# Optimization experiments

Measured on AMD Instinct MI355X. Metric: run time of the kernel, lower is better.

## Reference

```python
import jax, jax.numpy as jnp
import numpy as np

SHIFTS = (1, 2)          # _GLOBAL_SHIFTS, all < channels so none filtered
LN_EPS = 1e-5


def _layernorm(x, g, b):
    mu = jnp.mean(x, axis=-1, keepdims=True)
    var = jnp.var(x, axis=-1, keepdims=True)
    return (x - mu) * jax.lax.rsqrt(var + LN_EPS) * g + b


def setup_inputs() -> dict:
    key = jax.random.key(0)
    ks = jax.random.split(key, 4)
    B, H, W, D = 8, 96, 96, 256
    n_comp = 2 * len(SHIFTS)  # full mode: dot + wedge per shift
    x = jax.random.normal(ks[0], (B, H, W, D), dtype=jnp.float32)
    # glorot-uniform style scaling for the two dense kernels
    pk = jax.random.normal(ks[1], (n_comp * D, D), dtype=jnp.float32) * (1.0 / np.sqrt(n_comp * D))
    gk = jax.random.normal(ks[2], (2 * D, D), dtype=jnp.float32) * (1.0 / np.sqrt(2 * D))
    return {
        "x": x,
        "ln_gamma": jnp.ones((D,), jnp.float32),
        "ln_beta": jnp.zeros((D,), jnp.float32),
        "proj_kernel": pk,
        "proj_bias": jnp.zeros((D,), jnp.float32),
        "gate_kernel": gk,
        "gate_bias": jnp.zeros((D,), jnp.float32),
        "gamma": jnp.full((D,), 1e-5, jnp.float32),  # LayerScale init
    }


def reference(x, ln_gamma, ln_beta, proj_kernel, proj_bias,
              gate_kernel, gate_bias, gamma):
    # ---- pre-norm ----
    h_norm = _layernorm(x, ln_gamma, ln_beta)                 # [B,H,W,D]
    # ---- context stream (ctx_mode='diff'): deviation from spatial mean ----
    z_det = h_norm
    z_ctx = h_norm - jnp.mean(h_norm, axis=(1, 2), keepdims=True)
    # ---- sparse rolling Clifford product (cli_mode='full') ----
    feats = []
    for s in SHIFTS:
        ctx_s = jnp.roll(z_ctx, -s, axis=-1)   # Z_ctx[(c+s) % D]
        det_s = jnp.roll(z_det, -s, axis=-1)   # Z_det[(c+s) % D]
        dot = jax.nn.silu(z_det * ctx_s)                      # inner part
        wedge = z_det * ctx_s - z_ctx * det_s                 # bivector part
        feats.append(dot)
        feats.append(wedge)
    feats = jnp.concatenate(feats, axis=-1)                   # [B,H,W,4D]
    g_feat = feats @ proj_kernel + proj_bias                  # [B,H,W,D]
    # ---- gated geometric residual ----
    gate_in = jnp.concatenate([h_norm, g_feat], axis=-1)      # [B,H,W,2D]
    alpha = jax.nn.sigmoid(gate_in @ gate_kernel + gate_bias)
    h_mix = (jax.nn.silu(h_norm) + alpha * g_feat) * gamma    # LayerScale
    # drop_path_rate == 0.0 -> identity; caller-side residual add
    return x + h_mix
```

## Files before the change

### kernel.cpp

```cpp
#include <hip/hip_runtime.h>
#include <hip/hip_bf16.h>

typedef unsigned short u16;
typedef unsigned int   u32;
typedef __attribute__((ext_vector_type(2))) float f32x2;
typedef __attribute__((ext_vector_type(4))) float f32x4;
typedef __attribute__((ext_vector_type(4))) u32   u32x4;
typedef __attribute__((ext_vector_type(8))) short bf16x8;

#define HWPIX  9216
#define NPIX   73728
#define LN_EPS 1e-5f
#define MROW   64
#define ASTR   40

template<int N> struct IC { static constexpr int value = N; };

__device__ __forceinline__ u16 f2bf(float f){
  u32 u = __builtin_bit_cast(u32, f);
  u += 0x7fffu + ((u >> 16) & 1u);
  return (u16)(u >> 16);
}
__device__ __forceinline__ u32 pkbf(float lo, float hi){
  u32 d;
  asm("v_cvt_pk_bf16_f32 %0, %1, %2" : "=v"(d) : "v"(lo), "v"(hi));
  return d;
}
__device__ __forceinline__ float bfu2f(u16 h){ return __builtin_bit_cast(float, (u32)h << 16); }
__device__ __forceinline__ float fsigmoid(float v){ return __fdividef(1.f, 1.f + __expf(-v)); }
__device__ __forceinline__ float fsilu(float v){ return __fdividef(v, 1.f + __expf(-v)); }

__device__ __forceinline__ void gld16(const u16* g, u16* l){
  __builtin_amdgcn_global_load_lds((const __attribute__((address_space(1))) void*)g,
                                   (__attribute__((address_space(3))) void*)l,
                                   16, 0, 0);
}

__global__ __launch_bounds__(256) void wconv(const float* __restrict__ pk,
                                             const float* __restrict__ gk,
                                             u16* __restrict__ wsdot,
                                             u16* __restrict__ wsgate)
{
  int gid = blockIdx.x * 256 + threadIdx.x;
  int t = gid >> 10, S = gid & 1023;
  int q = (S >> 2) & 15, pp = S & 3, w8 = (S >> 6) & 7, rb = S >> 9;
  int n  = rb * 128 + w8 * 16 + q;
  int kq = pp ^ ((q >> 1) & 3);
  const float* W; int k0; u16* dst;
  if (t < 16) { W = pk; k0 = (t & 1) * 512 + (t >> 1) * 32 + kq * 8; dst = wsdot + (size_t)t * 8192; }
  else        { W = gk; k0 = (t - 16) * 32 + kq * 8;                 dst = wsgate + (size_t)(t - 16) * 8192; }
  u32 ow[4];
  #pragma unroll
  for (int e = 0; e < 4; ++e) {
    float f0 = W[(size_t)(k0 + 2*e)     * 256 + n];
    float f1 = W[(size_t)(k0 + 2*e + 1) * 256 + n];
    ow[e] = (u32)f2bf(f0) | ((u32)f2bf(f1) << 16);
  }
  *(u32x4*)(dst + (size_t)S * 8) = (u32x4){ow[0], ow[1], ow[2], ow[3]};
}

__global__ __launch_bounds__(256) void prep(const float* __restrict__ x,
                                            const float* __restrict__ g,
                                            const float* __restrict__ bt,
                                            float* __restrict__ mu_rs,
                                            float* __restrict__ partial)
{
  const int bh = blockIdx.x;
  const int tid = threadIdx.x;
  const int wv = tid >> 6, lane = tid & 63;
  const float* xrow = x + (size_t)bh * 96 * 256;
  __shared__ float red[4][256];

  f32x4 gv = *(const f32x4*)(g  + lane * 4);
  f32x4 bv = *(const f32x4*)(bt + lane * 4);
  f32x4 acc = {0.f, 0.f, 0.f, 0.f};

  for (int w = wv; w < 96; w += 4) {
    f32x4 v = *(const f32x4*)(xrow + w * 256 + lane * 4);
    float s  = v[0] + v[1] + v[2] + v[3];
    float s2 = v[0]*v[0] + v[1]*v[1] + v[2]*v[2] + v[3]*v[3];
    #pragma unroll
    for (int m = 1; m < 64; m <<= 1) { s += __shfl_xor(s, m); s2 += __shfl_xor(s2, m); }
    float mu  = s * (1.f / 256.f);
    float var = s2 * (1.f / 256.f) - mu * mu;
    float rs  = rsqrtf(var + LN_EPS);
    if (lane == 0) *(f32x2*)(mu_rs + (size_t)(bh * 96 + w) * 2) = f32x2{mu, rs};
    #pragma unroll
    for (int j = 0; j < 4; ++j) acc[j] += (v[j] - mu) * rs * gv[j] + bv[j];
  }
  *(f32x4*)(&red[wv][lane * 4]) = acc;
  __syncthreads();
  float s = red[0][tid] + red[1][tid] + red[2][tid] + red[3][tid];
  partial[(size_t)bh * 256 + tid] = s;
}

__global__ __launch_bounds__(256) void ln_mean(const float* __restrict__ partial,
                                               float* __restrict__ mean)
{
  int b = blockIdx.x, c = threadIdx.x;
  float s = 0.f;
  for (int h = 0; h < 96; ++h) s += partial[((size_t)b * 96 + h) * 256 + c];
  float m = s * (1.f / 9216.f);
  mean[b * 258 + c] = m;
  if (c < 2) mean[b * 258 + 256 + c] = m;
}

__global__ __launch_bounds__(256) void wfold(const float* __restrict__ pk,
                                             const float* __restrict__ meang,
                                             u16* __restrict__ wsW)
{
  __shared__ float msh[256];
  int gid = blockIdx.x * 256 + threadIdx.x;
  int chunk = gid >> 10;
  int b = chunk >> 3, j = chunk & 7;
  msh[threadIdx.x] = meang[b * 258 + threadIdx.x];
  __syncthreads();
  int S = gid & 1023;
  int q = (S >> 2) & 15, pp = S & 3, w8 = (S >> 6) & 7, rb = S >> 9;
  int n  = rb * 128 + w8 * 16 + q;
  int kq = pp ^ ((q >> 1) & 3);
  u32 ow[4];
  #pragma unroll
  for (int e = 0; e < 4; ++e) {
    float r[2];
    #pragma unroll
    for (int hh = 0; hh < 2; ++hh) {
      int c = j * 32 + kq * 8 + 2 * e + hh;
      int cm1 = (c + 255) & 255, cm2 = (c + 254) & 255;
      int cp1 = (c + 1) & 255,   cp2 = (c + 2) & 255;
      r[hh] = msh[cm1] * pk[(size_t)(256 + cm1) * 256 + n]
            - msh[cp1] * pk[(size_t)(256 + c)   * 256 + n]
            + msh[cm2] * pk[(size_t)(768 + cm2) * 256 + n]
            - msh[cp2] * pk[(size_t)(768 + c)   * 256 + n];
    }
    ow[e] = (u32)f2bf(r[0]) | ((u32)f2bf(r[1]) << 16);
  }
  *(u32x4*)(wsW + (size_t)chunk * 8192 + (size_t)S * 8) = (u32x4){ow[0], ow[1], ow[2], ow[3]};
}

__global__ __launch_bounds__(512, 2) void fused(
    const float* __restrict__ x,
    const float* __restrict__ lng, const float* __restrict__ lnb,
    const u16* __restrict__ wsdot, const u16* __restrict__ wsW,
    const u16* __restrict__ wsgate, const float* __restrict__ mu_rs,
    const float* __restrict__ pbias, const float* __restrict__ gbias,
    const float* __restrict__ gamma, const float* __restrict__ meang,
    float* __restrict__ out)
{
  __shared__ u16 afg[2][MROW * ASTR];
  __shared__ u16 Bl [4][8192];
  __shared__ float gshb[2][260];
  __shared__ float msh[258];
  __shared__ float mursh[128];

  const int tid  = threadIdx.x;
  const long pix0 = (long)blockIdx.x * MROW;
  const int bat  = (int)(pix0 / HWPIX);

  const int wave = tid >> 6, lane = tid & 63;
  const int wr = wave & 1, wc = wave >> 1;
  const int fr = lane & 15, kq = lane >> 4;
  const int bswz = (kq ^ ((fr >> 1) & 3)) * 8;
  const int brow = tid >> 3, o4 = (tid & 7) * 4;

  auto stageQ = [&](auto QC) {
    constexpr int q = decltype(QC)::value;
    constexpr int sl = q & 3;
    const u16* base;
    if constexpr (q < 32) {
      constexpr int w = q >> 2, r = q & 3;
      if constexpr      (r == 0) base = wsdot  + (size_t)(2 * w)     * 8192;
      else if constexpr (r == 1) base = wsdot  + (size_t)(2 * w + 1) * 8192;
      else if constexpr (r == 2) base = wsW + (size_t)bat * 65536 + (size_t)w * 8192;
      else                       base = wsgate + (size_t)w * 8192;
    } else {
      base = wsgate + (size_t)(q - 24) * 8192;
    }
    const u16* src = base + tid * 8;
    u16* dst = &Bl[sl][wave * 512];
    gld16(src, dst);
    gld16(src + 4096, dst + 4096);
  };

  stageQ(IC<0>{});
  stageQ(IC<1>{});

  if (tid < 256)      { gshb[0][tid] = lng[tid]; gshb[1][tid] = lnb[tid]; }
  else if (tid < 260) { int c = tid - 256; gshb[0][256 + c] = lng[c]; gshb[1][256 + c] = lnb[c]; }
  if (tid < 258) msh[tid] = meang[bat * 258 + tid];
  if (tid < 128) mursh[tid] = mu_rs[pix0 * 2 + tid];

  f32x4 accG[2][4], accA[2][4];
  #pragma unroll
  for (int i = 0; i < 2; ++i)
    #pragma unroll
    for (int j = 0; j < 4; ++j) { accG[i][j] = (f32x4){0,0,0,0}; accA[i][j] = (f32x4){0,0,0,0}; }
  u32 gfp[2][4][2];
  float pbv[4];
  #pragma unroll
  for (int nt = 0; nt < 4; ++nt) pbv[nt] = pbias[wc * 64 + nt * 16 + fr];

  __syncthreads();

  const float* xrowp = x + (pix0 + brow) * 256;
  const float muv = mursh[brow * 2];
  const float rsv = mursh[brow * 2 + 1];

  float h0, h1, h2, h3, h4, h5;
  auto computeH = [&](int w) {
    const int cc = w * 32 + o4;
    f32x4 xa = *(const f32x4*)(xrowp + cc);
    f32x2 xb = (cc == 252) ? f32x2{xrowp[0], xrowp[1]}
                           : *(const f32x2*)(xrowp + cc + 4);
    h0 = (xa[0] - muv) * rsv * gshb[0][cc]     + gshb[1][cc];
    h1 = (xa[1] - muv) * rsv * gshb[0][cc + 1] + gshb[1][cc + 1];
    h2 = (xa[2] - muv) * rsv * gshb[0][cc + 2] + gshb[1][cc + 2];
    h3 = (xa[3] - muv) * rsv * gshb[0][cc + 3] + gshb[1][cc + 3];
    h4 = (xb[0] - muv) * rsv * gshb[0][cc + 4] + gshb[1][cc + 4];
    h5 = (xb[1] - muv) * rsv * gshb[0][cc + 5] + gshb[1][cc + 5];
  };
  auto buildDot = [&](auto SC, int w, int buf) {
    constexpr int s = decltype(SC)::value;
    const int cc = w * 32 + o4;
    float a0, a1, a2, a3;
    if constexpr (s == 1) { a0 = h1; a1 = h2; a2 = h3; a3 = h4; }
    else                  { a0 = h2; a1 = h3; a2 = h4; a3 = h5; }
    float r0 = fsilu(h0 * (a0 - msh[cc + s]));
    float r1 = fsilu(h1 * (a1 - msh[cc + 1 + s]));
    float r2 = fsilu(h2 * (a2 - msh[cc + 2 + s]));
    float r3 = fsilu(h3 * (a3 - msh[cc + 3 + s]));
    *(u32*)(&afg[buf][brow * ASTR + o4])     = pkbf(r0, r1);
    *(u32*)(&afg[buf][brow * ASTR + o4 + 2]) = pkbf(r2, r3);
  };
  auto buildH = [&](int buf) {
    *(u32*)(&afg[buf][brow * ASTR + o4])     = pkbf(h0, h1);
    *(u32*)(&afg[buf][brow * ASTR + o4 + 2]) = pkbf(h2, h3);
  };
  auto gfcopy = [&](auto CGC, int buf) {
    constexpr int cg = decltype(CGC)::value;
    constexpr int par = cg & 1;
    if (wc == (cg >> 1)) {
      #pragma unroll
      for (int v = 0; v < 2; ++v) {
        #pragma unroll
        for (int ai = 0; ai < 2; ++ai)
          #pragma unroll
          for (int rp = 0; rp < 2; ++rp) {
            u32 pw = gfp[ai][par * 2 + v][rp];
            int row0 = wr * 32 + ai * 16 + kq * 4 + rp * 2;
            afg[buf][row0 * ASTR + v * 16 + fr]       = (u16)pw;
            afg[buf][(row0 + 1) * ASTR + v * 16 + fr] = (u16)(pw >> 16);
          }
      }
    }
  };

  auto mfma_into = [&](f32x4 (&ac)[2][4], int abuf, const u16* bp) {
    const u16* ar = &afg[abuf][(wr * 32 + fr) * ASTR + kq * 8];
    bf16x8 av0 = *(const bf16x8*)(ar);
    bf16x8 av1 = *(const bf16x8*)(ar + 16 * ASTR);
    __builtin_amdgcn_s_setprio(1);
    #pragma unroll
    for (int nt = 0; nt < 4; ++nt) {
      bf16x8 bv = *(const bf16x8*)(bp + nt * 512);
      ac[0][nt] = __builtin_amdgcn_mfma_f32_16x16x32_bf16(av0, bv, ac[0][nt], 0, 0, 0);
      ac[1][nt] = __builtin_amdgcn_mfma_f32_16x16x32_bf16(av1, bv, ac[1][nt], 0, 0, 0);
    }
    __builtin_amdgcn_s_setprio(0);
  };

  computeH(0);
  buildDot(IC<1>{}, 0, 0);
  asm volatile("s_waitcnt lgkmcnt(0)" ::: "memory");
  __builtin_amdgcn_s_barrier();

  auto stepfn = [&](auto TC) {
    constexpr int t = decltype(TC)::value;
    constexpr int u = t + 1;
    if constexpr (u < 24) {
      constexpr int r3 = u % 3, w = u / 3;
      if constexpr (r3 == 0)      { computeH(w); buildDot(IC<1>{}, w, u & 1); }
      else if constexpr (r3 == 1) buildDot(IC<2>{}, u / 3, u & 1);
      else                        buildH(u & 1);
    } else if constexpr (u >= 25 && u < 32) {
      gfcopy(IC<u - 24>{}, u & 1);
    }
    if constexpr (t < 24) {
      constexpr int g = t / 3, r3 = t % 3;
      if constexpr (r3 < 2) {
        constexpr int q = 4 * g + r3;
        mfma_into(accG, t & 1, &Bl[q & 3][wc * 2048 + fr * 32 + bswz]);
      } else {
        constexpr int q = 4 * g + 2;
        mfma_into(accG, t & 1, &Bl[q & 3][wc * 2048 + fr * 32 + bswz]);
        mfma_into(accA, t & 1, &Bl[(q + 1) & 3][wc * 2048 + fr * 32 + bswz]);
      }
    } else {
      constexpr int q = t + 8;
      mfma_into(accA, t & 1, &Bl[q & 3][wc * 2048 + fr * 32 + bswz]);
    }
    if constexpr (t == 23) {
      #pragma unroll
      for (int nt = 0; nt < 4; ++nt)
        #pragma unroll
        for (int ai = 0; ai < 2; ++ai) {
          f32x4 a = accG[ai][nt];
          gfp[ai][nt][0] = pkbf(a[0] + pbv[nt], a[1] + pbv[nt]);
          gfp[ai][nt][1] = pkbf(a[2] + pbv[nt], a[3] + pbv[nt]);
        }
      gfcopy(IC<0>{}, 0);
    }
    if constexpr (t + 2 < 32) {
      constexpr int s2 = t + 2;
      constexpr int nq = (s2 < 24) ? ((s2 % 3 == 2) ? 2 : 1) : 1;
      constexpr int q0 = (s2 < 24) ? (4 * (s2 / 3) + s2 % 3) : (s2 + 8);
      stageQ(IC<q0>{});
      if constexpr (nq == 2) {
        stageQ(IC<q0 + 1>{});
        asm volatile("s_waitcnt vmcnt(4) lgkmcnt(0)" ::: "memory");
      } else {
        asm volatile("s_waitcnt vmcnt(2) lgkmcnt(0)" ::: "memory");
      }
    } else {
      asm volatile("s_waitcnt vmcnt(0) lgkmcnt(0)" ::: "memory");
    }
    __builtin_amdgcn_s_barrier();
  };
  auto run8 = [&](auto B8) {
    constexpr int b8 = decltype(B8)::value;
    stepfn(IC<b8 + 0>{}); stepfn(IC<b8 + 1>{}); stepfn(IC<b8 + 2>{}); stepfn(IC<b8 + 3>{});
    stepfn(IC<b8 + 4>{}); stepfn(IC<b8 + 5>{}); stepfn(IC<b8 + 6>{}); stepfn(IC<b8 + 7>{});
  };
  run8(IC<0>{}); run8(IC<8>{}); run8(IC<16>{}); run8(IC<24>{});

  float gbv[4], gmv[4];
  #pragma unroll
  for (int nt = 0; nt < 4; ++nt) {
    int col = wc * 64 + nt * 16 + fr;
    gbv[nt] = gbias[col]; gmv[nt] = gamma[col];
  }
  #pragma unroll
  for (int ai = 0; ai < 2; ++ai)
    #pragma unroll
    for (int rr = 0; rr < 4; ++rr) {
      const int row = wr * 32 + ai * 16 + kq * 4 + rr;
      const long pix = pix0 + row;
      const float mu2 = mursh[row * 2], rs2 = mursh[row * 2 + 1];
      #pragma unroll
      for (int nt = 0; nt < 4; ++nt) {
        int col = wc * 64 + nt * 16 + fr;
        float xv = x[pix * 256 + col];
        float hh = (xv - mu2) * rs2 * gshb[0][col] + gshb[1][col];
        u32 pw = gfp[ai][nt][rr >> 1];
        float gfv = bfu2f((u16)((rr & 1) ? (pw >> 16) : pw));
        float al = fsigmoid(accA[ai][nt][rr] + gbv[nt]);
        out[pix * 256 + col] = xv + (fsilu(hh) + al * gfv) * gmv[nt];
      }
    }
}

extern "C" void kernel_launch(void* const* d_in, const int* in_sizes, int n_in,
                              void* d_out, int out_size, void* d_ws, size_t ws_size,
                              hipStream_t stream) {
  const float* x     = (const float*)d_in[0];
  const float* lng   = (const float*)d_in[1];
  const float* lnb   = (const float*)d_in[2];
  const float* pk    = (const float*)d_in[3];
  const float* pbias = (const float*)d_in[4];
  const float* gk    = (const float*)d_in[5];
  const float* gbias = (const float*)d_in[6];
  const float* gamma = (const float*)d_in[7];
  float* out = (float*)d_out;

  char* ws = (char*)d_ws;
  u16*   wsdot   = (u16*)ws;
  u16*   wsgate  = (u16*)(ws + 262144);
  float* meang   = (float*)(ws + 524288);
  u16*   wsW     = (u16*)(ws + 532544);
  float* partial = (float*)(ws + 532544);
  float* mu_rs   = (float*)(ws + 1581120);

  wconv<<<128, 256, 0, stream>>>(pk, gk, wsdot, wsgate);
  prep<<<768, 256, 0, stream>>>(x, lng, lnb, mu_rs, partial);
  ln_mean<<<8, 256, 0, stream>>>(partial, meang);
  wfold<<<256, 256, 0, stream>>>(pk, meang, wsW);
  fused<<<NPIX / MROW, 512, 0, stream>>>(x, lng, lnb, wsdot, wsW, wsgate, mu_rs,
                                         pbias, gbias, gamma, meang, out);
}
```

Baseline: 164.0 us.

## Reorder GEMM K-loop into uniform one-chunk steps with a triple-buffered weight ring

The fused K-loop is restructured so that every step stages and consumes exactly one 8192-element weight chunk. All dot chunks run first, then alternating wedge/gate-h chunks, then the remaining gate chunks. The LDS weight ring shrinks from four slots to three, and the step count grows from 32 to 40 with a uniform vmcnt(2) wait. Because channel chunks are now visited twice, the LayerNorm values for the gate-h chunks are recomputed from x via a new computeH4. This adds extra global reads and more barriers in exchange for a simpler, lower-LDS pipeline.

```diff
diff --git a/kernel.cpp b/kernel.cpp
--- a/kernel.cpp
+++ b/kernel.cpp
@@ -148,7 +148,7 @@
     float* __restrict__ out)
 {
   __shared__ u16 afg[2][MROW * ASTR];
-  __shared__ u16 Bl [4][8192];
+  __shared__ u16 Bl [3][8192];
   __shared__ float gshb[2][260];
   __shared__ float msh[258];
   __shared__ float mursh[128];
@@ -164,15 +164,15 @@
   const int brow = tid >> 3, o4 = (tid & 7) * 4;
 
   auto stageQ = [&](auto QC) {
-    constexpr int q = decltype(QC)::value;
-    constexpr int sl = q & 3;
+    constexpr int q  = decltype(QC)::value;
+    constexpr int sl = q % 3;
     const u16* base;
-    if constexpr (q < 32) {
-      constexpr int w = q >> 2, r = q & 3;
-      if constexpr      (r == 0) base = wsdot  + (size_t)(2 * w)     * 8192;
-      else if constexpr (r == 1) base = wsdot  + (size_t)(2 * w + 1) * 8192;
-      else if constexpr (r == 2) base = wsW + (size_t)bat * 65536 + (size_t)w * 8192;
-      else                       base = wsgate + (size_t)w * 8192;
+    if constexpr (q < 16) {
+      base = wsdot + (size_t)q * 8192;
+    } else if constexpr (q < 32) {
+      constexpr int p = q - 16, w = p >> 1;
+      if constexpr ((p & 1) == 0) base = wsW + (size_t)bat * 65536 + (size_t)w * 8192;
+      else                        base = wsgate + (size_t)w * 8192;
     } else {
       base = wsgate + (size_t)(q - 24) * 8192;
     }
@@ -196,9 +196,6 @@
     #pragma unroll
     for (int j = 0; j < 4; ++j) { accG[i][j] = (f32x4){0,0,0,0}; accA[i][j] = (f32x4){0,0,0,0}; }
   u32 gfp[2][4][2];
-  float pbv[4];
-  #pragma unroll
-  for (int nt = 0; nt < 4; ++nt) pbv[nt] = pbias[wc * 64 + nt * 16 + fr];
 
   __syncthreads();
 
@@ -207,7 +204,7 @@
   const float rsv = mursh[brow * 2 + 1];
 
   float h0, h1, h2, h3, h4, h5;
-  auto computeH = [&](int w) {
+  auto computeH6 = [&](int w) {
     const int cc = w * 32 + o4;
     f32x4 xa = *(const f32x4*)(xrowp + cc);
     f32x2 xb = (cc == 252) ? f32x2{xrowp[0], xrowp[1]}
@@ -218,6 +215,14 @@
     h3 = (xa[3] - muv) * rsv * gshb[0][cc + 3] + gshb[1][cc + 3];
     h4 = (xb[0] - muv) * rsv * gshb[0][cc + 4] + gshb[1][cc + 4];
     h5 = (xb[1] - muv) * rsv * gshb[0][cc + 5] + gshb[1][cc + 5];
+  };
+  auto computeH4 = [&](int w) {
+    const int cc = w * 32 + o4;
+    f32x4 xa = *(const f32x4*)(xrowp + cc);
+    h0 = (xa[0] - muv) * rsv * gshb[0][cc]     + gshb[1][cc];
+    h1 = (xa[1] - muv) * rsv * gshb[0][cc + 1] + gshb[1][cc + 1];
+    h2 = (xa[2] - muv) * rsv * gshb[0][cc + 2] + gshb[1][cc + 2];
+    h3 = (xa[3] - muv) * rsv * gshb[0][cc + 3] + gshb[1][cc + 3];
   };
   auto buildDot = [&](auto SC, int w, int buf) {
     constexpr int s = decltype(SC)::value;
@@ -255,10 +260,11 @@
     }
   };
 
-  auto mfma_into = [&](f32x4 (&ac)[2][4], int abuf, const u16* bp) {
+  auto mfma_into = [&](f32x4 (&ac)[2][4], int abuf, int sl) {
     const u16* ar = &afg[abuf][(wr * 32 + fr) * ASTR + kq * 8];
     bf16x8 av0 = *(const bf16x8*)(ar);
     bf16x8 av1 = *(const bf16x8*)(ar + 16 * ASTR);
+    const u16* bp = &Bl[sl][wc * 2048 + fr * 32 + bswz];
     __builtin_amdgcn_s_setprio(1);
     #pragma unroll
     for (int nt = 0; nt < 4; ++nt) {
@@ -269,7 +275,7 @@
     __builtin_amdgcn_s_setprio(0);
   };
 
-  computeH(0);
+  computeH6(0);
   buildDot(IC<1>{}, 0, 0);
   asm volatile("s_waitcnt lgkmcnt(0)" ::: "memory");
   __builtin_amdgcn_s_barrier();
@@ -277,53 +283,44 @@
   auto stepfn = [&](auto TC) {
     constexpr int t = decltype(TC)::value;
     constexpr int u = t + 1;
-    if constexpr (u < 24) {
-      constexpr int r3 = u % 3, w = u / 3;
-      if constexpr (r3 == 0)      { computeH(w); buildDot(IC<1>{}, w, u & 1); }
-      else if constexpr (r3 == 1) buildDot(IC<2>{}, u / 3, u & 1);
-      else                        buildH(u & 1);
-    } else if constexpr (u >= 25 && u < 32) {
-      gfcopy(IC<u - 24>{}, u & 1);
-    }
-    if constexpr (t < 24) {
-      constexpr int g = t / 3, r3 = t % 3;
-      if constexpr (r3 < 2) {
-        constexpr int q = 4 * g + r3;
-        mfma_into(accG, t & 1, &Bl[q & 3][wc * 2048 + fr * 32 + bswz]);
-      } else {
-        constexpr int q = 4 * g + 2;
-        mfma_into(accG, t & 1, &Bl[q & 3][wc * 2048 + fr * 32 + bswz]);
-        mfma_into(accA, t & 1, &Bl[(q + 1) & 3][wc * 2048 + fr * 32 + bswz]);
+    if constexpr (u < 16) {
+      constexpr int w = u >> 1;
+      if constexpr ((u & 1) == 0) { computeH6(w); buildDot(IC<1>{}, w, u & 1); }
+      else                        buildDot(IC<2>{}, w, u & 1);
+    } else if constexpr (u >= 16 && u < 32) {
+      if constexpr (((u - 16) & 1) == 0) {
+        constexpr int p = (u - 16) >> 1;
+        computeH4(p);
+        buildH(p & 1);
       }
+    } else if constexpr (u >= 33 && u < 40) {
+      gfcopy(IC<u - 32>{}, u & 1);
+    }
+    if constexpr (t < 16) {
+      mfma_into(accG, t & 1, t % 3);
+    } else if constexpr (t < 32) {
+      constexpr int p = (t - 16) >> 1;
+      if constexpr (((t - 16) & 1) == 0) mfma_into(accG, p & 1, t % 3);
+      else                               mfma_into(accA, p & 1, t % 3);
     } else {
-      constexpr int q = t + 8;
-      mfma_into(accA, t & 1, &Bl[q & 3][wc * 2048 + fr * 32 + bswz]);
-    }
-    if constexpr (t == 23) {
+      mfma_into(accA, t & 1, t % 3);
+    }
+    if constexpr (t == 31) {
       #pragma unroll
-      for (int nt = 0; nt < 4; ++nt)
+      for (int nt = 0; nt < 4; ++nt) {
+        float pb = pbias[wc * 64 + nt * 16 + fr];
         #pragma unroll
         for (int ai = 0; ai < 2; ++ai) {
           f32x4 a = accG[ai][nt];
-          gfp[ai][nt][0] = pkbf(a[0] + pbv[nt], a[1] + pbv[nt]);
-          gfp[ai][nt][1] = pkbf(a[2] + pbv[nt], a[3] + pbv[nt]);
+          gfp[ai][nt][0] = pkbf(a[0] + pb, a[1] + pb);
+          gfp[ai][nt][1] = pkbf(a[2] + pb, a[3] + pb);
         }
+      }
       gfcopy(IC<0>{}, 0);
     }
-    if constexpr (t + 2 < 32) {
-      constexpr int s2 = t + 2;
-      constexpr int nq = (s2 < 24) ? ((s2 % 3 == 2) ? 2 : 1) : 1;
-      constexpr int q0 = (s2 < 24) ? (4 * (s2 / 3) + s2 % 3) : (s2 + 8);
-      stageQ(IC<q0>{});
-      if constexpr (nq == 2) {
-        stageQ(IC<q0 + 1>{});
-        asm volatile("s_waitcnt vmcnt(4) lgkmcnt(0)" ::: "memory");
-      } else {
-        asm volatile("s_waitcnt vmcnt(2) lgkmcnt(0)" ::: "memory");
-      }
-    } else {
-      asm volatile("s_waitcnt vmcnt(0) lgkmcnt(0)" ::: "memory");
-    }
+    if constexpr (t + 2 < 40) stageQ(IC<t + 2>{});
+    if constexpr (t < 37) asm volatile("s_waitcnt vmcnt(2) lgkmcnt(0)" ::: "memory");
+    else                  asm volatile("s_waitcnt vmcnt(0) lgkmcnt(0)" ::: "memory");
     __builtin_amdgcn_s_barrier();
   };
   auto run8 = [&](auto B8) {
@@ -331,7 +328,7 @@
     stepfn(IC<b8 + 0>{}); stepfn(IC<b8 + 1>{}); stepfn(IC<b8 + 2>{}); stepfn(IC<b8 + 3>{});
     stepfn(IC<b8 + 4>{}); stepfn(IC<b8 + 5>{}); stepfn(IC<b8 + 6>{}); stepfn(IC<b8 + 7>{});
   };
-  run8(IC<0>{}); run8(IC<8>{}); run8(IC<16>{}); run8(IC<24>{});
+  run8(IC<0>{}); run8(IC<8>{}); run8(IC<16>{}); run8(IC<24>{}); run8(IC<32>{});
 
   float gbv[4], gmv[4];
   #pragma unroll
```

After: 138.4 us. -15.6%, faster.
